# Performance work log

Measured on AMD Instinct MI355X. Metric: run time of the kernel, lower is better.

## Reference

```python
import jax, jax.numpy as jnp
import numpy as np

B, C, H, W = 64, 64, 32, 32
K, D = 1024, 64
COMMITMENT_COST = 0.25


def setup_inputs() -> dict:
    key = jax.random.key(0)
    k1, k2 = jax.random.split(key)
    x = jax.random.normal(k1, (B, C, H, W), dtype=jnp.float32)
    # torch init: uniform(-1/codebook_size, 1/codebook_size)
    embedding = jax.random.uniform(k2, (K, D), dtype=jnp.float32,
                                   minval=-1.0 / K, maxval=1.0 / K)
    return {"x": x, "embedding": embedding}


def reference(x, embedding):
    k, d = embedding.shape
    xt = jnp.transpose(x, (0, 2, 3, 1))          # [B, H, W, D]
    flat = xt.reshape(-1, d)                     # [N, D]
    x_sq = jnp.sum(flat * flat, axis=1, keepdims=True)        # [N, 1]
    e_sq = jnp.sum(embedding * embedding, axis=1)              # [K]
    distances = (x_sq - 2.0 * flat @ embedding.T + e_sq) / d   # [N, K]
    encoding_indices = jnp.argmin(distances, axis=1)           # [N]
    quantized = embedding[encoding_indices].reshape(xt.shape)  # [B, H, W, D]
    e_latent_loss = jnp.mean((jax.lax.stop_gradient(quantized) - xt) ** 2)
    q_latent_loss = jnp.mean((quantized - jax.lax.stop_gradient(xt)) ** 2)
    loss = q_latent_loss + COMMITMENT_COST * e_latent_loss
    # straight-through estimator (training mode)
    quantized = xt + jax.lax.stop_gradient(quantized - xt)
    return (loss,
            jnp.transpose(quantized, (0, 3, 1, 2)),            # [B, C, H, W]
            encoding_indices.reshape(x.shape[0], -1))          # [B, H*W]
```

## Files before the change

kernel.cpp:

```cpp
#include <hip/hip_runtime.h>


#define KCODES 1024
#define DDIM   64
#define NPIX   65536
#define QELEMS 4194304
#define IDX_OFF (1 + QELEMS)
#define MARGIN 8e-5f
#define WT     4
#define NWIN   16
#define NB     8
#define NCLEAN 512

typedef __attribute__((ext_vector_type(8))) short bf16x8;
typedef __attribute__((ext_vector_type(4))) float f32x4;

static __device__ __forceinline__ unsigned short f2bf(float f) {
    unsigned int u = __float_as_uint(f);
    unsigned int r = (u + 0x7FFFu + ((u >> 16) & 1u)) >> 16;
    return (unsigned short)r;
}
static __device__ __forceinline__ float bf2f(unsigned short h) {
    return __uint_as_float(((unsigned int)h) << 16);
}

__global__ void __launch_bounds__(256) esplit_kernel(const float* __restrict__ e,
                                                     float* __restrict__ esq,
                                                     unsigned short* __restrict__ Eh,
                                                     unsigned short* __restrict__ El,
                                                     int* __restrict__ count,
                                                     float* __restrict__ dpart) {
    const int gid = blockIdx.x * 256 + threadIdx.x;
    if (gid == 0) *count = 0;
    if (gid < NCLEAN) dpart[gid] = 0.f;

    const int k = gid;
    if (k >= KCODES) return;
    const float* row = e + k * DDIM;
    {
#pragma clang fp contract(off)
        float r[8];
#pragma unroll
        for (int j = 0; j < 8; ++j) r[j] = row[j] * row[j];
#pragma unroll
        for (int i = 1; i < 8; ++i) {
#pragma unroll
            for (int j = 0; j < 8; ++j) { float v = row[i * 8 + j]; r[j] += v * v; }
        }
        esq[k] = ((r[0] + r[1]) + (r[2] + r[3])) + ((r[4] + r[5]) + (r[6] + r[7]));
    }
#pragma unroll
    for (int d = 0; d < DDIM; ++d) {
        float v = -2.0f * row[d];
        unsigned short h = f2bf(v);
        Eh[k * DDIM + d] = h;
        El[k * DDIM + d] = f2bf(v - bf2f(h));
    }
}

__global__ void __launch_bounds__(256, 4) gemm_kernel(const float* __restrict__ x,
                                                      const float* __restrict__ e,
                                                      const unsigned short* __restrict__ Eh,
                                                      const unsigned short* __restrict__ El,
                                                      const float* __restrict__ esq,
                                                      int* __restrict__ count,
                                                      int* __restrict__ list,
                                                      float* __restrict__ partial,
                                                      float* __restrict__ out) {
    __shared__ float x_lds[DDIM][64];
    __shared__ float esq_lds[KCODES];
    __shared__ unsigned char btile[2][WT][4096];
    __shared__ int sflag[64];
    __shared__ int sidx_l[64];

    const int tid = threadIdx.x;
    const int w = __builtin_amdgcn_readfirstlane(tid >> 6);
    const int l = tid & 63;
    const int g = l >> 4;
    const int col = l & 15;
    const int pxbase = blockIdx.x * 64;
    const int b = pxbase >> 10;
    const int p0 = pxbase & 1023;

    {
        const float* xg = x + (size_t)b * 65536 + p0;
        for (int t = tid; t < DDIM * 64; t += 256)
            x_lds[t >> 6][t & 63] = xg[(size_t)(t >> 6) * 1024 + (t & 63)];
        for (int t = tid; t < KCODES; t += 256)
            esq_lds[t] = esq[t];
    }
    __syncthreads();

    bf16x8 Ah0, Ah1, Al0, Al1;
    {
        const int pxl = w * 16 + col;
#pragma unroll
        for (int j = 0; j < 8; ++j) {
            float v0 = x_lds[g * 8 + j][pxl];
            unsigned short h0 = f2bf(v0);
            Ah0[j] = (short)h0;
            Al0[j] = (short)f2bf(v0 - bf2f(h0));
            float v1 = x_lds[32 + g * 8 + j][pxl];
            unsigned short h1 = f2bf(v1);
            Ah1[j] = (short)h1;
            Al1[j] = (short)f2bf(v1 - bf2f(h1));
        }
    }

    const unsigned short* src_base = (tid < 128) ? Eh : El;
    const int u = tid & 127;
    const int code_w = u >> 3;
    const int dst_off = ((tid >> 7) << 11) + (code_w << 7)
                      + (((u & 7) << 4) ^ ((code_w & 7) << 4));
    float4 s0g, s1g, s2g, s3g;
    auto LDW = [&](int i) {
        const char* sb = (const char*)src_base + (size_t)(4 * i) * 2048 + (size_t)u * 16;
        s0g = *(const float4*)(sb);
        s1g = *(const float4*)(sb + 2048);
        s2g = *(const float4*)(sb + 4096);
        s3g = *(const float4*)(sb + 6144);
    };
    auto STW = [&](int i) {
        *(float4*)&btile[i & 1][0][dst_off] = s0g;
        *(float4*)&btile[i & 1][1][dst_off] = s1g;
        *(float4*)&btile[i & 1][2][dst_off] = s2g;
        *(float4*)&btile[i & 1][3][dst_off] = s3g;
    };

    const int cx = (col & 7) << 4;
    const int rb = col << 7;
    const int oh0 = rb + ((g << 4) ^ cx);
    const int oh1 = rb + (((g << 4) + 64) ^ cx);

    float m1_0 = 3.4e38f, m1_1 = 3.4e38f, m1_2 = 3.4e38f, m1_3 = 3.4e38f;
    float m2_0 = 3.4e38f, m2_1 = 3.4e38f, m2_2 = 3.4e38f, m2_3 = 3.4e38f;
    int i1_0 = 0, i1_1 = 0, i1_2 = 0, i1_3 = 0;

    LDW(0); STW(0);
    LDW(1);
    __syncthreads();

#pragma unroll 1
    for (int wn = 0; wn < NWIN; ++wn) {
        if (wn + 1 < NWIN) STW(wn + 1);
        if (wn + 2 < NWIN) LDW(wn + 2);

        const unsigned char* bw = &btile[wn & 1][0][0];
        const int kbase = wn * 64 + col;

        f32x4 t0, t1, t2, t3;
#define CHAIN(J, ACC)                                                          \
        {                                                                      \
            const unsigned char* bp_ = bw + (J) * 4096;                        \
            const bf16x8 Bh0 = *(const bf16x8*)(bp_ + oh0);                    \
            const bf16x8 Bh1 = *(const bf16x8*)(bp_ + oh1);                    \
            const bf16x8 Bl0 = *(const bf16x8*)(bp_ + 2048 + oh0);             \
            const bf16x8 Bl1 = *(const bf16x8*)(bp_ + 2048 + oh1);             \
            const float qe_ = esq_lds[kbase + (J) * 16];                       \
            ACC = (f32x4){qe_, qe_, qe_, qe_};                                 \
            ACC = __builtin_amdgcn_mfma_f32_16x16x32_bf16(Ah0, Bh0, ACC, 0, 0, 0); \
            ACC = __builtin_amdgcn_mfma_f32_16x16x32_bf16(Al0, Bh0, ACC, 0, 0, 0); \
            ACC = __builtin_amdgcn_mfma_f32_16x16x32_bf16(Ah0, Bl0, ACC, 0, 0, 0); \
            ACC = __builtin_amdgcn_mfma_f32_16x16x32_bf16(Ah1, Bh1, ACC, 0, 0, 0); \
            ACC = __builtin_amdgcn_mfma_f32_16x16x32_bf16(Al1, Bh1, ACC, 0, 0, 0); \
            ACC = __builtin_amdgcn_mfma_f32_16x16x32_bf16(Ah1, Bl1, ACC, 0, 0, 0); \
        }
        CHAIN(0, t0)
        CHAIN(1, t1)
        CHAIN(2, t2)
        CHAIN(3, t3)
#undef CHAIN

#define WTOP(R, M1, M2, I1)                                                    \
        {                                                                      \
            float s0_ = t0[R], s1_ = t1[R], s2_ = t2[R], s3_ = t3[R];          \
            float p01 = fminf(s0_, s1_), q01 = fmaxf(s0_, s1_);                \
            float p23 = fminf(s2_, s3_), q23 = fmaxf(s2_, s3_);                \
            int i01 = (s1_ < s0_) ? kbase + 16 : kbase;                        \
            int i23 = (s3_ < s2_) ? kbase + 48 : kbase + 32;                   \
            float wmin = fminf(p01, p23);                                      \
            float wsec = fminf(fminf(q01, q23), fmaxf(p01, p23));              \
            int wi = (p23 < p01) ? i23 : i01;                                  \
            M2 = fminf(M2, fminf(wsec, fmaxf(M1, wmin)));                      \
            if (wmin < M1) I1 = wi;                                            \
            M1 = fminf(M1, wmin);                                              \
        }
        WTOP(0, m1_0, m2_0, i1_0)
        WTOP(1, m1_1, m2_1, i1_1)
        WTOP(2, m1_2, m2_2, i1_2)
        WTOP(3, m1_3, m2_3, i1_3)
#undef WTOP
        __syncthreads();
    }

#define MERGE(M1, M2, I1, R)                                                   \
    {                                                                          \
        float a1_ = M1, a2_ = M2; int j1 = I1;                                 \
        _Pragma("unroll")                                                      \
        for (int off = 1; off < 16; off <<= 1) {                               \
            float b1 = __shfl_xor(a1_, off);                                   \
            int jb = __shfl_xor(j1, off);                                      \
            float b2 = __shfl_xor(a2_, off);                                   \
            float hi = fmaxf(a1_, b1);                                         \
            a2_ = fminf(fminf(a2_, b2), hi);                                   \
            if (b1 < a1_) j1 = jb;                                             \
            a1_ = fminf(a1_, b1);                                              \
        }                                                                      \
        if (col == 0) {                                                        \
            int pxl = w * 16 + g * 4 + (R);                                    \
            sflag[pxl] = (a2_ <= a1_ + MARGIN) ? 1 : 0;                        \
            sidx_l[pxl] = j1;                                                  \
        }                                                                      \
    }
    MERGE(m1_0, m2_0, i1_0, 0)
    MERGE(m1_1, m2_1, i1_1, 1)
    MERGE(m1_2, m2_2, i1_2, 2)
    MERGE(m1_3, m2_3, i1_3, 3)
#undef MERGE

    __syncthreads();

    if (tid < 64) {
        out[IDX_OFF + pxbase + tid] = (float)sidx_l[tid];
        const bool f = sflag[tid] != 0;
        unsigned long long m = __ballot(f);
        int base = 0;
        if (l == 0 && m) base = atomicAdd(count, __popcll(m));
        base = __shfl(base, 0);
        if (f) {
            unsigned long long below = m & ((1ULL << l) - 1ULL);
            list[base + __popcll(below)] = pxbase + tid;
        }
    }

    {
        const int px = tid & 63;
        const int dc = (tid >> 6) << 4;
        const int j1 = sidx_l[px];
        const bool fl = sflag[px] != 0;
        const float* er = e + (size_t)j1 * DDIM + dc;
        const float4 e0v = *(const float4*)(er);
        const float4 e1v = *(const float4*)(er + 4);
        const float4 e2v = *(const float4*)(er + 8);
        const float4 e3v = *(const float4*)(er + 12);
        float* ob = out + 1 + (((size_t)(b * 64 + dc)) << 10) + p0 + px;
        float acc = 0.f;
#define QW(VV, I0)                                                             \
        {                                                                      \
            ob[(size_t)(I0 + 0) << 10] = VV.x;                                 \
            ob[(size_t)(I0 + 1) << 10] = VV.y;                                 \
            ob[(size_t)(I0 + 2) << 10] = VV.z;                                 \
            ob[(size_t)(I0 + 3) << 10] = VV.w;                                 \
            float d0_ = VV.x - x_lds[dc + I0 + 0][px];                         \
            float d1_ = VV.y - x_lds[dc + I0 + 1][px];                         \
            float d2_ = VV.z - x_lds[dc + I0 + 2][px];                         \
            float d3_ = VV.w - x_lds[dc + I0 + 3][px];                         \
            acc = __builtin_fmaf(d0_, d0_, acc);                               \
            acc = __builtin_fmaf(d1_, d1_, acc);                               \
            acc = __builtin_fmaf(d2_, d2_, acc);                               \
            acc = __builtin_fmaf(d3_, d3_, acc);                               \
        }
        QW(e0v, 0)
        QW(e1v, 4)
        QW(e2v, 8)
        QW(e3v, 12)
#undef QW
        if (fl) acc = 0.f;
        __syncthreads();
        float* red = &x_lds[0][0];
        red[tid] = acc;
        __syncthreads();
        for (int s = 128; s > 0; s >>= 1) {
            if (tid < s) red[tid] += red[tid + s];
            __syncthreads();
        }
        if (tid == 0) partial[blockIdx.x] = red[0];
    }
}

__global__ void __launch_bounds__(256, 4) cleanup_kernel(const float* __restrict__ x,
                                                         const float* __restrict__ e,
                                                         const float* __restrict__ esq,
                                                         const int* __restrict__ count,
                                                         const int* __restrict__ list,
                                                         float* __restrict__ dpart,
                                                         float* __restrict__ out) {
    __shared__ float tile[DDIM][257];
    __shared__ float xs[NB][68];
    __shared__ float xsqs[NB];
    __shared__ float rbest[4];
    __shared__ int   ridx[4];
    __shared__ int   plist[NB];
    __shared__ int   jsel;
    __shared__ float dacc;

    const int tid = threadIdx.x;
    const int cnt = *count;
    const int nchunk = (cnt + NB - 1) / NB;
    if (tid == 0) dacc = 0.f;

    for (int chunk = blockIdx.x; chunk < nchunk; chunk += gridDim.x) {
        const int base = chunk * NB;
        const int np = min(NB, cnt - base);

        if (tid < np) plist[tid] = list[base + tid];
        __syncthreads();
        for (int q = tid; q < np * 64; q += 256) {
            const int pp = q >> 6, d = q & 63;
            const int p = plist[pp];
            xs[pp][d] = x[(size_t)(p >> 10) * 65536 + (size_t)d * 1024 + (p & 1023)];
        }
        __syncthreads();
        if (tid < np) {
#pragma clang fp contract(off)
            float r[8];
#pragma unroll
            for (int j = 0; j < 8; ++j) { float v = xs[tid][j]; r[j] = v * v; }
#pragma unroll
            for (int ii = 1; ii < 8; ++ii) {
#pragma unroll
                for (int j = 0; j < 8; ++j) { float v = xs[tid][ii * 8 + j]; r[j] += v * v; }
            }
            xsqs[tid] = ((r[0] + r[1]) + (r[2] + r[3])) + ((r[4] + r[5]) + (r[6] + r[7]));
        }

        float best[NB];
        int bidx[NB];
#pragma unroll
        for (int pp = 0; pp < NB; ++pp) { best[pp] = 3.4e38f; bidx[pp] = 0; }

#pragma unroll 1
        for (int T = 0; T < 4; ++T) {
            __syncthreads();
#pragma unroll
            for (int i = 0; i < 16; ++i) {
                const float4 v = *(const float4*)(e + (size_t)T * 16384 + (size_t)i * 1024 + tid * 4);
                const int c = 16 * i + (tid >> 4);
                const int d0 = (4 * tid) & 63;
                tile[d0 + 0][c] = v.x;
                tile[d0 + 1][c] = v.y;
                tile[d0 + 2][c] = v.z;
                tile[d0 + 3][c] = v.w;
            }
            __syncthreads();
            const float qe = esq[T * 256 + tid];
            const int kk = T * 256 + tid;
#pragma unroll
            for (int pp = 0; pp < NB; ++pp) {
                if (pp < np) {
                    float dt = 0.f;
#pragma unroll
                    for (int d = 0; d < DDIM; ++d)
                        dt = __builtin_fmaf(xs[pp][d], tile[d][tid], dt);
                    const float s = (xsqs[pp] - 2.0f * dt) + qe;
                    if (s < best[pp]) { best[pp] = s; bidx[pp] = kk; }
                }
            }
        }

#pragma unroll
        for (int pp = 0; pp < NB; ++pp) {
            if (pp < np) {
                const int p = plist[pp];
                float bb = best[pp];
                int bj = bidx[pp];
#pragma unroll
                for (int off = 1; off < 64; off <<= 1) {
                    float b2 = __shfl_xor(bb, off);
                    int k2 = __shfl_xor(bj, off);
                    if (b2 < bb || (b2 == bb && k2 < bj)) { bb = b2; bj = k2; }
                }
                if ((tid & 63) == 0) { rbest[tid >> 6] = bb; ridx[tid >> 6] = bj; }
                __syncthreads();
                if (tid == 0) {
                    float b0 = rbest[0]; int j0 = ridx[0];
#pragma unroll
                    for (int c2 = 1; c2 < 4; ++c2)
                        if (rbest[c2] < b0 || (rbest[c2] == b0 && ridx[c2] < j0)) {
                            b0 = rbest[c2]; j0 = ridx[c2];
                        }
                    jsel = j0;
                    out[IDX_OFF + p] = (float)j0;
                }
                __syncthreads();
                if (tid < 64) {
                    const int j0 = jsel;
                    const int d = tid;
                    const float ev = e[(size_t)j0 * DDIM + d];
                    const float xv = xs[pp][d];
                    out[1 + (((size_t)((p >> 10) * 64 + d)) << 10) + (p & 1023)] = ev;
                    float df = ev - xv;
                    float c = df * df;
#pragma unroll
                    for (int off = 1; off < 64; off <<= 1)
                        c += __shfl_xor(c, off);
                    if (tid == 0) dacc += c;
                }
                __syncthreads();
            }
        }
        __syncthreads();
    }
    if (tid == 0) dpart[blockIdx.x] = dacc;
}

__global__ void __launch_bounds__(256) loss_kernel(const float* __restrict__ partial,
                                                   const float* __restrict__ dpart,
                                                   float* __restrict__ out) {
    float acc = 0.f;
    for (int i = threadIdx.x; i < 1024; i += 256) acc += partial[i];
    for (int i = threadIdx.x; i < NCLEAN; i += 256) acc += dpart[i];
    __shared__ float sm[256];
    sm[threadIdx.x] = acc;
    __syncthreads();
    for (int s = 128; s > 0; s >>= 1) {
        if (threadIdx.x < s) sm[threadIdx.x] += sm[threadIdx.x + s];
        __syncthreads();
    }
    if (threadIdx.x == 0) out[0] = sm[0] * (1.25f / 4194304.f);
}

extern "C" void kernel_launch(void* const* d_in, const int* in_sizes, int n_in,
                              void* d_out, int out_size, void* d_ws, size_t ws_size,
                              hipStream_t stream) {
    const float* x = (const float*)d_in[0];
    const float* e = (const float*)d_in[1];
    float* out = (float*)d_out;

    char* wsb = (char*)d_ws;
    float*          esq     = (float*)wsb;
    unsigned short* Eh      = (unsigned short*)(wsb + 4096);
    unsigned short* El      = (unsigned short*)(wsb + 4096 + 131072);
    int*            count   = (int*)(wsb + 4096 + 2 * 131072);
    int*            list    = (int*)(wsb + 4096 + 2 * 131072 + 4096);
    float*          partial = (float*)(wsb + 4096 + 2 * 131072 + 4096 + NPIX * 4);
    float*          dpart   = (float*)(wsb + 4096 + 2 * 131072 + 4096 + NPIX * 4 + 4096);

    esplit_kernel<<<16, 256, 0, stream>>>(e, esq, Eh, El, count, dpart);
    gemm_kernel<<<NPIX / 64, 256, 0, stream>>>(x, e, Eh, El, esq, count, list, partial, out);
    cleanup_kernel<<<NCLEAN, 256, 0, stream>>>(x, e, esq, count, list, dpart, out);
    loss_kernel<<<1, 256, 0, stream>>>(partial, dpart, out);
}
```

Measured before the change: 96.08 us.

## Parallelize codebook split via LDS and shrink GEMM code window to 32

The codebook preprocessing kernel now runs 64 blocks, each staging 16 codes through shared memory with coalesced float4 loads and vectorized bf16 hi/lo stores, instead of one thread per code doing strided scalar work. The GEMM kernel halves the code tile per window (WT 2, NWIN 32), which halves the LDS B-tile and staging registers and shortens the per-window top-2 reduction. The aim is a faster serial prologue kernel and a smaller LDS and register footprint for higher occupancy. The cost is twice as many window iterations and barriers in the main loop.

Result: faster. 89.68 us (-6.7%).

```diff
diff --git a/kernel.cpp b/kernel.cpp
--- a/kernel.cpp
+++ b/kernel.cpp
@@ -7,8 +7,8 @@
 #define QELEMS 4194304
 #define IDX_OFF (1 + QELEMS)
 #define MARGIN 8e-5f
-#define WT     4
-#define NWIN   16
+#define WT     2
+#define NWIN   32
 #define NB     8
 #define NCLEAN 512
 
@@ -30,31 +30,51 @@
                                                      unsigned short* __restrict__ El,
                                                      int* __restrict__ count,
                                                      float* __restrict__ dpart) {
-    const int gid = blockIdx.x * 256 + threadIdx.x;
-    if (gid == 0) *count = 0;
-    if (gid < NCLEAN) dpart[gid] = 0.f;
-
-    const int k = gid;
-    if (k >= KCODES) return;
-    const float* row = e + k * DDIM;
+    __shared__ float se[16][64];
+    const int tid = threadIdx.x;
+    const int bk = blockIdx.x;
+    if (bk == 0) {
+        if (tid == 0) *count = 0;
+        for (int i = tid; i < NCLEAN; i += 256) dpart[i] = 0.f;
+    }
+
     {
+        const float4 v = *(const float4*)(e + (size_t)bk * 1024 + tid * 4);
+        const int c = tid >> 4;
+        const int d0 = (tid & 15) * 4;
+        se[c][d0 + 0] = v.x;
+        se[c][d0 + 1] = v.y;
+        se[c][d0 + 2] = v.z;
+        se[c][d0 + 3] = v.w;
+    }
+    __syncthreads();
+
+    if (tid < 16) {
 #pragma clang fp contract(off)
         float r[8];
 #pragma unroll
-        for (int j = 0; j < 8; ++j) r[j] = row[j] * row[j];
+        for (int j = 0; j < 8; ++j) { float v = se[tid][j]; r[j] = v * v; }
 #pragma unroll
         for (int i = 1; i < 8; ++i) {
 #pragma unroll
-            for (int j = 0; j < 8; ++j) { float v = row[i * 8 + j]; r[j] += v * v; }
-        }
-        esq[k] = ((r[0] + r[1]) + (r[2] + r[3])) + ((r[4] + r[5]) + (r[6] + r[7]));
-    }
-#pragma unroll
-    for (int d = 0; d < DDIM; ++d) {
-        float v = -2.0f * row[d];
-        unsigned short h = f2bf(v);
-        Eh[k * DDIM + d] = h;
-        El[k * DDIM + d] = f2bf(v - bf2f(h));
+            for (int j = 0; j < 8; ++j) { float v = se[tid][i * 8 + j]; r[j] += v * v; }
+        }
+        esq[bk * 16 + tid] = ((r[0] + r[1]) + (r[2] + r[3])) + ((r[4] + r[5]) + (r[6] + r[7]));
+    }
+
+    {
+        const int c = tid >> 4;
+        const int d0 = (tid & 15) * 4;
+        unsigned short h[4], lo[4];
+#pragma unroll
+        for (int j = 0; j < 4; ++j) {
+            float v = -2.0f * se[c][d0 + j];
+            h[j] = f2bf(v);
+            lo[j] = f2bf(v - bf2f(h[j]));
+        }
+        const size_t off = (size_t)(bk * 16 + c) * DDIM + d0;
+        *(ushort4*)(Eh + off) = make_ushort4(h[0], h[1], h[2], h[3]);
+        *(ushort4*)(El + off) = make_ushort4(lo[0], lo[1], lo[2], lo[3]);
     }
 }
 
@@ -112,19 +132,15 @@
     const int code_w = u >> 3;
     const int dst_off = ((tid >> 7) << 11) + (code_w << 7)
                       + (((u & 7) << 4) ^ ((code_w & 7) << 4));
-    float4 s0g, s1g, s2g, s3g;
+    float4 s0g, s1g;
     auto LDW = [&](int i) {
-        const char* sb = (const char*)src_base + (size_t)(4 * i) * 2048 + (size_t)u * 16;
+        const char* sb = (const char*)src_base + (size_t)(2 * i) * 2048 + (size_t)u * 16;
         s0g = *(const float4*)(sb);
         s1g = *(const float4*)(sb + 2048);
-        s2g = *(const float4*)(sb + 4096);
-        s3g = *(const float4*)(sb + 6144);
     };
     auto STW = [&](int i) {
         *(float4*)&btile[i & 1][0][dst_off] = s0g;
         *(float4*)&btile[i & 1][1][dst_off] = s1g;
-        *(float4*)&btile[i & 1][2][dst_off] = s2g;
-        *(float4*)&btile[i & 1][3][dst_off] = s3g;
     };
 
     const int cx = (col & 7) << 4;
@@ -146,9 +162,9 @@
         if (wn + 2 < NWIN) LDW(wn + 2);
 
         const unsigned char* bw = &btile[wn & 1][0][0];
-        const int kbase = wn * 64 + col;
-
-        f32x4 t0, t1, t2, t3;
+        const int kbase = wn * 32 + col;
+
+        f32x4 t0, t1;
 #define CHAIN(J, ACC)                                                          \
         {                                                                      \
             const unsigned char* bp_ = bw + (J) * 4096;                        \
@@ -167,23 +183,16 @@
         }
         CHAIN(0, t0)
         CHAIN(1, t1)
-        CHAIN(2, t2)
-        CHAIN(3, t3)
 #undef CHAIN
 
 #define WTOP(R, M1, M2, I1)                                                    \
         {                                                                      \
-            float s0_ = t0[R], s1_ = t1[R], s2_ = t2[R], s3_ = t3[R];          \
+            float s0_ = t0[R], s1_ = t1[R];                                    \
             float p01 = fminf(s0_, s1_), q01 = fmaxf(s0_, s1_);                \
-            float p23 = fminf(s2_, s3_), q23 = fmaxf(s2_, s3_);                \
             int i01 = (s1_ < s0_) ? kbase + 16 : kbase;                        \
-            int i23 = (s3_ < s2_) ? kbase + 48 : kbase + 32;                   \
-            float wmin = fminf(p01, p23);                                      \
-            float wsec = fminf(fminf(q01, q23), fmaxf(p01, p23));              \
-            int wi = (p23 < p01) ? i23 : i01;                                  \
-            M2 = fminf(M2, fminf(wsec, fmaxf(M1, wmin)));                      \
-            if (wmin < M1) I1 = wi;                                            \
-            M1 = fminf(M1, wmin);                                              \
+            M2 = fminf(M2, fminf(q01, fmaxf(M1, p01)));                        \
+            if (p01 < M1) I1 = i01;                                            \
+            M1 = fminf(M1, p01);                                               \
         }
         WTOP(0, m1_0, m2_0, i1_0)
         WTOP(1, m1_1, m2_1, i1_1)
@@ -436,7 +445,7 @@
     float*          partial = (float*)(wsb + 4096 + 2 * 131072 + 4096 + NPIX * 4);
     float*          dpart   = (float*)(wsb + 4096 + 2 * 131072 + 4096 + NPIX * 4 + 4096);
 
-    esplit_kernel<<<16, 256, 0, stream>>>(e, esq, Eh, El, count, dpart);
+    esplit_kernel<<<64, 256, 0, stream>>>(e, esq, Eh, El, count, dpart);
     gemm_kernel<<<NPIX / 64, 256, 0, stream>>>(x, e, Eh, El, esq, count, list, partial, out);
     cleanup_kernel<<<NCLEAN, 256, 0, stream>>>(x, e, esq, count, list, dpart, out);
     loss_kernel<<<1, 256, 0, stream>>>(partial, dpart, out);
```
